# Kernel tuning notes

Hardware: AMD Instinct MI355X
Metric: run time of the kernel (lower is better)

The kernel has to match this reference:

```python
import jax, jax.numpy as jnp
import numpy as np

TAU = 0.5  # config.tau
EPS = 1e-12  # F.normalize eps


def _pair_idx(n_i, hi):
    # all pairs (i, j) with i in [0, n_i), j in (i, hi)
    ii, jj = [], []
    for i in range(n_i):
        js = np.arange(i + 1, hi)
        ii.append(np.full(js.shape, i))
        jj.append(js)
    return np.concatenate(ii), np.concatenate(jj)


def setup_inputs() -> dict:
    key = jax.random.key(0)
    ks = jax.random.split(key, 7)
    B, D, H = 512, 768, 256
    s = 0.02
    return {
        "emb_in": jax.random.normal(ks[0], (B, D), jnp.float32),
        "W1": jax.random.normal(ks[1], (H, 2 * D), jnp.float32) * s,
        "b1": jax.random.normal(ks[2], (H,), jnp.float32) * s,
        "W2": jax.random.normal(ks[3], (H, H), jnp.float32) * s,
        "b2": jax.random.normal(ks[4], (H,), jnp.float32) * s,
        "W3": jax.random.normal(ks[5], (1, H), jnp.float32) * s,
        "b3": jax.random.normal(ks[6], (1,), jnp.float32) * s,
    }


def reference(emb_in, W1, b1, W2, b2, W3, b3):
    B, D = emb_in.shape
    n = B // 4
    m = B // 2

    # L2 normalize rows (torch F.normalize)
    z = emb_in / jnp.maximum(jnp.linalg.norm(emb_in, axis=1, keepdims=True), EPS)
    # cosine similarity matrix [B, B]
    S = z @ z.T

    # ---- ContrastiveLoss (NT-Xent style over first n rows) ----
    logits = S / jnp.asarray(TAU, emb_in.dtype)
    not_diag = 1.0 - jnp.eye(B, dtype=emb_in.dtype)
    denom = jnp.sum(not_diag * jnp.exp(logits), axis=1)  # sum_{k != i} exp(S[i,k]/T)
    log_denom = jnp.log(denom)  # [B]
    ci, cj = _pair_idx(n, n)  # pairs i < j < n
    # loss_ij = -log( exp(S[i,j]/T) / denom_i ) = log_denom[i] - logits[i, j]
    closs_sum = jnp.sum(log_denom[ci] - logits[ci, cj])
    closs = (-2.0 * (n - 1) / n) * closs_sum

    # ---- en_loss: pairwise concat + tiny MLP + BCEWithLogits ----
    ei_np, ej_np = _pair_idx(n, B)  # pairs i in [0,n), j in (i, B)
    ei = jnp.asarray(ei_np)
    ej = jnp.asarray(ej_np)
    labels = (ej_np < m).astype(np.float32)  # first m-(i+1) pairs per i are positives
    labels = jnp.asarray(labels)

    x = jnp.concatenate([z[ei], z[ej]], axis=1)  # [P, 2D]
    h1 = jax.nn.relu(x @ W1.T + b1)              # [P, H]
    h2 = jax.nn.relu(h1 @ W2.T + b2)             # [P, H]
    logit = (h2 @ W3.T + b3)[:, 0]               # [P]

    # BCEWithLogitsLoss (mean), numerically stable form
    bce = jnp.maximum(logit, 0.0) - logit * labels + jnp.log1p(jnp.exp(-jnp.abs(logit)))
    eloss = jnp.mean(bce)

    return closs + eloss
```

## Files before the change

### kernel.cpp

```cpp
#include <hip/hip_runtime.h>
#include <hip/hip_bf16.h>
#include <math.h>

#define B 512
#define D 768
#define H 256
#define NN 128
#define MM 256
#define P_PAIRS 57280
#define NPBLK_P 448

typedef _Float16 f16x8 __attribute__((ext_vector_type(8)));
typedef _Float16 f16x4 __attribute__((ext_vector_type(4)));
typedef float f32x4 __attribute__((ext_vector_type(4)));


__global__ __launch_bounds__(256) void k_prep(const float* __restrict__ emb,
                                              const float* __restrict__ W1,
                                              const float* __restrict__ W2,
                                              _Float16* __restrict__ zH,
                                              _Float16* __restrict__ W1H,
                                              _Float16* __restrict__ W2H) {
    int bx = blockIdx.x;
    int tid = threadIdx.x;
    int w = tid >> 6, lane = tid & 63;

    if (bx < 32) {
        int g = bx;
        __shared__ float invs[16];
        for (int rr = 0; rr < 4; rr++) {
            int row = 16 * g + 4 * w + rr;
            const float* rp = emb + row * D;
            float ss = 0.f;
            #pragma unroll
            for (int it = 0; it < 12; it++) {
                float v = rp[lane + 64 * it];
                ss += v * v;
            }
            #pragma unroll
            for (int m = 1; m <= 32; m <<= 1) ss += __shfl_xor(ss, m);
            if (lane == 0) invs[4 * w + rr] = 1.0f / fmaxf(sqrtf(ss), 1e-12f);
        }
        __syncthreads();
        for (int it = 0; it < 6; it++) {
            int chunk = it * 256 + tid;
            int s = chunk >> 6, lc = chunk & 63;
            int q = lc >> 4, r = lc & 15;
            const float* src = emb + (16 * g + r) * D + 32 * s + 8 * q;
            float inv = invs[r];
            float4 a = *(const float4*)src;
            float4 b = *(const float4*)(src + 4);
            f16x8 o;
            o[0] = (_Float16)(a.x * inv); o[1] = (_Float16)(a.y * inv);
            o[2] = (_Float16)(a.z * inv); o[3] = (_Float16)(a.w * inv);
            o[4] = (_Float16)(b.x * inv); o[5] = (_Float16)(b.y * inv);
            o[6] = (_Float16)(b.z * inv); o[7] = (_Float16)(b.w * inv);
            *(f16x8*)(zH + ((g * 24 + s) * 64 + lc) * 8) = o;
        }
    } else if (bx < 64) {
        int g = bx - 32;
        for (int it = 0; it < 6; it++) {
            int chunk = it * 256 + tid;
            int s = chunk >> 6, lc = chunk & 63;
            int q = lc >> 4, r = lc & 15;
            int n = 16 * g + r;
            const float* src = W1 + (n & 255) * (2 * D) + (n >> 8) * D + 32 * s + 8 * q;
            float4 a = *(const float4*)src;
            float4 b = *(const float4*)(src + 4);
            f16x8 o;
            o[0] = (_Float16)a.x; o[1] = (_Float16)a.y; o[2] = (_Float16)a.z; o[3] = (_Float16)a.w;
            o[4] = (_Float16)b.x; o[5] = (_Float16)b.y; o[6] = (_Float16)b.z; o[7] = (_Float16)b.w;
            *(f16x8*)(W1H + ((g * 24 + s) * 64 + lc) * 8) = o;
        }
    } else {
        int g = bx - 64;
        for (int it = 0; it < 2; it++) {
            int chunk = it * 256 + tid;
            int s = chunk >> 6, lc = chunk & 63;
            int q = lc >> 4, r = lc & 15;
            const float* src = W2 + (16 * g + r) * H + 32 * s + 8 * q;
            float4 a = *(const float4*)src;
            float4 b = *(const float4*)(src + 4);
            f16x8 o;
            o[0] = (_Float16)a.x; o[1] = (_Float16)a.y; o[2] = (_Float16)a.z; o[3] = (_Float16)a.w;
            o[4] = (_Float16)b.x; o[5] = (_Float16)b.y; o[6] = (_Float16)b.z; o[7] = (_Float16)b.w;
            *(f16x8*)(W2H + ((g * 8 + s) * 64 + lc) * 8) = o;
        }
    }
}

__global__ __launch_bounds__(256) void k_uv(const _Float16* __restrict__ zH,
                                            const _Float16* __restrict__ W1H,
                                            const float* __restrict__ b1,
                                            _Float16* __restrict__ Up,
                                            _Float16* __restrict__ Vv) {
    int w = threadIdx.x >> 6;
    int lane = threadIdx.x & 63;
    int r = lane & 15, q = lane >> 4;
    int tile = blockIdx.x * 4 + w;
    int gm = tile >> 4;
    int gnp = tile & 15;

    f32x4 acc[2] = {};
    #pragma unroll 4
    for (int s = 0; s < 24; s++) {
        f16x8 a = *(const f16x8*)(zH + ((gm * 24 + s) * 64 + lane) * 8);
        #pragma unroll
        for (int nt = 0; nt < 2; nt++) {
            f16x8 b = *(const f16x8*)(W1H + (((gnp * 2 + nt) * 24 + s) * 64 + lane) * 8);
            acc[nt] = __builtin_amdgcn_mfma_f32_16x16x32_f16(a, b, acc[nt], 0, 0, 0);
        }
    }
    #pragma unroll
    for (int nt = 0; nt < 2; nt++) {
        int n = (gnp * 2 + nt) * 16 + r;
        float bias = (n < H) ? b1[n] : 0.f;
        #pragma unroll
        for (int rr = 0; rr < 4; rr++) {
            int m = gm * 16 + 4 * q + rr;
            float C = acc[nt][rr] + bias;
            if (n < H) Up[m * H + n] = (_Float16)C;
            else       Vv[m * H + (n - H)] = (_Float16)C;
        }
    }
}

__global__ __launch_bounds__(256, 2) void k_pairs(const _Float16* __restrict__ Up,
                                                  const _Float16* __restrict__ Vv,
                                                  const _Float16* __restrict__ W2H,
                                                  const _Float16* __restrict__ zH,
                                                  const float* __restrict__ b2,
                                                  const float* __restrict__ W3,
                                                  const float* __restrict__ b3,
                                                  float* __restrict__ bcepart,
                                                  float* __restrict__ esp,
                                                  float* __restrict__ slp) {
    int tid = threadIdx.x;
    int w = tid >> 6, lane = tid & 63;
    int r = lane & 15, q = lane >> 4;
    int bx = blockIdx.x;

    if (bx >= NPBLK_P) {
        int t = (bx - NPBLK_P) * 4 + w;
        int gm = t >> 3;
        int slot = t & 7;
        int gn0 = slot * 4;
        f32x4 acc[4] = {};
        #pragma unroll 4
        for (int s = 0; s < 24; s++) {
            f16x8 a = *(const f16x8*)(zH + ((gm * 24 + s) * 64 + lane) * 8);
            #pragma unroll
            for (int nt = 0; nt < 4; nt++) {
                f16x8 b = *(const f16x8*)(zH + (((gn0 + nt) * 24 + s) * 64 + lane) * 8);
                acc[nt] = __builtin_amdgcn_mfma_f32_16x16x32_f16(a, b, acc[nt], 0, 0, 0);
            }
        }
        #pragma unroll
        for (int rr = 0; rr < 4; rr++) {
            int irow = gm * 16 + q * 4 + rr;
            float es = 0.f, sl = 0.f;
            #pragma unroll
            for (int nt = 0; nt < 4; nt++) {
                int kcol = (gn0 + nt) * 16 + r;
                float C = acc[nt][rr];
                if (kcol != irow) es += expf(2.f * C);
                if (kcol > irow && kcol < NN) sl += 2.f * C;
            }
            #pragma unroll
            for (int m = 1; m <= 8; m <<= 1) {
                es += __shfl_xor(es, m);
                sl += __shfl_xor(sl, m);
            }
            if (r == 0) {
                esp[slot * NN + irow] = es;
                slp[slot * NN + irow] = sl;
            }
        }
        return;
    }

    __shared__ _Float16 h1[128][264];
    __shared__ int jj_s[128];
    __shared__ float redbuf[4][128];
    __shared__ float red2[2];

    int p0 = bx * 128;
    if (tid < 128) {
        int p = p0 + tid;
        if (p >= P_PAIRS) p = P_PAIRS - 1;
        float disc = 1046529.f - 8.f * (float)p;
        int i = (int)((1023.f - sqrtf(disc)) * 0.5f);
        if (i < 0) i = 0;
        if (i > NN - 1) i = NN - 1;
        while (i > 0 && i * (1023 - i) / 2 > p) i--;
        while ((i + 1) * (1022 - i) / 2 <= p) i++;
        int j = i + 1 + (p - i * (1023 - i) / 2);
        jj_s[tid] = (i << 16) | j;
    }
    __syncthreads();

    {
        #pragma unroll
        for (int uu = 0; uu < 2; uu++) {
            int u = uu * 256 + tid;
            int row = u >> 2, cq = u & 3;
            int ij = jj_s[row];
            int i = ij >> 16, j = ij & 0xffff;
            const _Float16* up = Up + i * H + 64 * cq;
            const _Float16* vp = Vv + j * H + 64 * cq;
            #pragma unroll
            for (int c8 = 0; c8 < 8; c8++) {
                f16x8 u8 = *(const f16x8*)(up + 8 * c8);
                f16x8 v8 = *(const f16x8*)(vp + 8 * c8);
                f16x8 zero = {};
                f16x8 hv = __builtin_elementwise_max(u8 + v8, zero);
                *(f16x8*)&h1[row][64 * cq + 8 * c8] = hv;
            }
        }
    }
    __syncthreads();

    f32x4 acc[8][4] = {};
    #pragma unroll
    for (int s = 0; s < 8; s++) {
        f16x8 b[4];
        #pragma unroll
        for (int nt = 0; nt < 4; nt++)
            b[nt] = *(const f16x8*)(W2H + (((4 * w + nt) * 8 + s) * 64 + lane) * 8);
        #pragma unroll
        for (int mt = 0; mt < 8; mt++) {
            f16x8 a = *(const f16x8*)&h1[16 * mt + r][32 * s + 8 * q];
            #pragma unroll
            for (int nt = 0; nt < 4; nt++)
                acc[mt][nt] = __builtin_amdgcn_mfma_f32_16x16x32_f16(a, b[nt], acc[mt][nt], 0, 0, 0);
        }
    }

    float b2v[4], w3v[4];
    #pragma unroll
    for (int nt = 0; nt < 4; nt++) {
        int n = 64 * w + 16 * nt + r;
        b2v[nt] = b2[n];
        w3v[nt] = W3[n];
    }
    #pragma unroll
    for (int mt = 0; mt < 8; mt++) {
        float part[4] = {0.f, 0.f, 0.f, 0.f};
        #pragma unroll
        for (int nt = 0; nt < 4; nt++)
            #pragma unroll
            for (int rr = 0; rr < 4; rr++) {
                float h2 = fmaxf(acc[mt][nt][rr] + b2v[nt], 0.f);
                part[rr] += h2 * w3v[nt];
            }
        #pragma unroll
        for (int rr = 0; rr < 4; rr++) {
            float v = part[rr];
            #pragma unroll
            for (int m = 1; m <= 8; m <<= 1) v += __shfl_xor(v, m);
            if (r == 0) redbuf[w][16 * mt + 4 * q + rr] = v;
        }
    }
    __syncthreads();

    if (tid < 128) {
        int p = p0 + tid;
        int j = jj_s[tid] & 0xffff;
        float lsum = 0.f;
        if (p < P_PAIRS) {
            float logit = redbuf[0][tid] + redbuf[1][tid] +
                          redbuf[2][tid] + redbuf[3][tid] + b3[0];
            float label = (j < MM) ? 1.f : 0.f;
            lsum = fmaxf(logit, 0.f) - logit * label + log1pf(expf(-fabsf(logit)));
        }
        #pragma unroll
        for (int off = 32; off > 0; off >>= 1) lsum += __shfl_down(lsum, off);
        if ((tid & 63) == 0) red2[tid >> 6] = lsum;
    }
    __syncthreads();
    if (tid == 0) bcepart[bx] = red2[0] + red2[1];
}

__global__ __launch_bounds__(256) void k_final(const float* __restrict__ esp,
                                               const float* __restrict__ slp,
                                               const float* __restrict__ bcepart,
                                               float* __restrict__ out) {
    __shared__ float red[256];
    int t = threadIdx.x;

    float s = 0.f;
    for (int p = t; p < NPBLK_P; p += 256) s += bcepart[p];
    red[t] = s;
    __syncthreads();
    for (int st = 128; st > 0; st >>= 1) {
        if (t < st) red[t] += red[t + st];
        __syncthreads();
    }
    float bce_total = red[0];
    __syncthreads();

    float v = 0.f;
    if (t < NN) {
        float es = 0.f, sl = 0.f;
        #pragma unroll
        for (int s8 = 0; s8 < 8; s8++) {
            es += esp[s8 * NN + t];
            sl += slp[s8 * NN + t];
        }
        v = (float)(NN - 1 - t) * logf(es) - sl;
    }
    red[t] = v;
    __syncthreads();
    for (int st = 128; st > 0; st >>= 1) {
        if (t < st) red[t] += red[t + st];
        __syncthreads();
    }
    if (t == 0) {
        float closs = (-2.0f * (float)(NN - 1) / (float)NN) * red[0];
        out[0] = closs + bce_total / (float)P_PAIRS;
    }
}

extern "C" void kernel_launch(void* const* d_in, const int* in_sizes, int n_in,
                              void* d_out, int out_size, void* d_ws, size_t ws_size,
                              hipStream_t stream) {
    const float* emb = (const float*)d_in[0];
    const float* W1  = (const float*)d_in[1];
    const float* b1  = (const float*)d_in[2];
    const float* W2  = (const float*)d_in[3];
    const float* b2  = (const float*)d_in[4];
    const float* W3  = (const float*)d_in[5];
    const float* b3  = (const float*)d_in[6];
    float* out = (float*)d_out;

    float* ws = (float*)d_ws;
    float* esp     = ws;
    float* slp     = ws + 1024;
    float* bcepart = ws + 2048;
    _Float16* zH  = (_Float16*)(ws + 2560);
    _Float16* W1H = zH + B * D;
    _Float16* W2H = W1H + 2 * H * D;
    _Float16* Up  = W2H + H * H;
    _Float16* Vv  = Up + B * H;

    k_prep<<<80, 256, 0, stream>>>(emb, W1, W2, zH, W1H, W2H);
    k_uv<<<128, 256, 0, stream>>>(zH, W1H, b1, Up, Vv);
    k_pairs<<<NPBLK_P + 16, 256, 0, stream>>>(Up, Vv, W2H, zH, b2, W3, b3,
                                              bcepart, esp, slp);
    k_final<<<1, 256, 0, stream>>>(esp, slp, bcepart, out);
}
```

Baseline: 101.3 us.

## Fuse fp16 conversion into GEMM loads, move similarity GEMM earlier, fold final reduction

```diff
diff --git a/kernel.cpp b/kernel.cpp
--- a/kernel.cpp
+++ b/kernel.cpp
@@ -11,74 +11,43 @@
 #define NPBLK_P 448
 
 typedef _Float16 f16x8 __attribute__((ext_vector_type(8)));
-typedef _Float16 f16x4 __attribute__((ext_vector_type(4)));
 typedef float f32x4 __attribute__((ext_vector_type(4)));
 
 
-__global__ __launch_bounds__(256) void k_prep(const float* __restrict__ emb,
-                                              const float* __restrict__ W1,
+__global__ __launch_bounds__(256) void k_norm(const float* __restrict__ emb,
                                               const float* __restrict__ W2,
-                                              _Float16* __restrict__ zH,
-                                              _Float16* __restrict__ W1H,
-                                              _Float16* __restrict__ W2H) {
+                                              float* __restrict__ inv,
+                                              _Float16* __restrict__ W2H,
+                                              int* __restrict__ counter) {
     int bx = blockIdx.x;
-    int tid = threadIdx.x;
-    int w = tid >> 6, lane = tid & 63;
-
+    int t = threadIdx.x;
     if (bx < 32) {
-        int g = bx;
-        __shared__ float invs[16];
-        for (int rr = 0; rr < 4; rr++) {
-            int row = 16 * g + 4 * w + rr;
-            const float* rp = emb + row * D;
-            float ss = 0.f;
-            #pragma unroll
-            for (int it = 0; it < 12; it++) {
-                float v = rp[lane + 64 * it];
-                ss += v * v;
-            }
-            #pragma unroll
-            for (int m = 1; m <= 32; m <<= 1) ss += __shfl_xor(ss, m);
-            if (lane == 0) invs[4 * w + rr] = 1.0f / fmaxf(sqrtf(ss), 1e-12f);
-        }
+        __shared__ float ssq[16][17];
+        int row16 = t >> 4, seg = t & 15;
+        const float4* rp = (const float4*)(emb + (16 * bx + row16) * D + seg * 48);
+        float ss = 0.f;
+        #pragma unroll
+        for (int it = 0; it < 12; it++) {
+            float4 v = rp[it];
+            ss += v.x * v.x + v.y * v.y + v.z * v.z + v.w * v.w;
+        }
+        ssq[row16][seg] = ss;
         __syncthreads();
-        for (int it = 0; it < 6; it++) {
-            int chunk = it * 256 + tid;
+        if (t < 16) {
+            float s = 0.f;
+            #pragma unroll
+            for (int k = 0; k < 16; k++) s += ssq[t][k];
+            inv[16 * bx + t] = 1.0f / fmaxf(sqrtf(s), 1e-12f);
+        }
+    } else {
+        int g = bx - 32;
+        if (g == 0 && t == 0) *counter = 0;
+        #pragma unroll
+        for (int it = 0; it < 2; it++) {
+            int chunk = it * 256 + t;
             int s = chunk >> 6, lc = chunk & 63;
-            int q = lc >> 4, r = lc & 15;
-            const float* src = emb + (16 * g + r) * D + 32 * s + 8 * q;
-            float inv = invs[r];
-            float4 a = *(const float4*)src;
-            float4 b = *(const float4*)(src + 4);
-            f16x8 o;
-            o[0] = (_Float16)(a.x * inv); o[1] = (_Float16)(a.y * inv);
-            o[2] = (_Float16)(a.z * inv); o[3] = (_Float16)(a.w * inv);
-            o[4] = (_Float16)(b.x * inv); o[5] = (_Float16)(b.y * inv);
-            o[6] = (_Float16)(b.z * inv); o[7] = (_Float16)(b.w * inv);
-            *(f16x8*)(zH + ((g * 24 + s) * 64 + lc) * 8) = o;
-        }
-    } else if (bx < 64) {
-        int g = bx - 32;
-        for (int it = 0; it < 6; it++) {
-            int chunk = it * 256 + tid;
-            int s = chunk >> 6, lc = chunk & 63;
-            int q = lc >> 4, r = lc & 15;
-            int n = 16 * g + r;
-            const float* src = W1 + (n & 255) * (2 * D) + (n >> 8) * D + 32 * s + 8 * q;
-            float4 a = *(const float4*)src;
-            float4 b = *(const float4*)(src + 4);
-            f16x8 o;
-            o[0] = (_Float16)a.x; o[1] = (_Float16)a.y; o[2] = (_Float16)a.z; o[3] = (_Float16)a.w;
-            o[4] = (_Float16)b.x; o[5] = (_Float16)b.y; o[6] = (_Float16)b.z; o[7] = (_Float16)b.w;
-            *(f16x8*)(W1H + ((g * 24 + s) * 64 + lc) * 8) = o;
-        }
-    } else {
-        int g = bx - 64;
-        for (int it = 0; it < 2; it++) {
-            int chunk = it * 256 + tid;
-            int s = chunk >> 6, lc = chunk & 63;
-            int q = lc >> 4, r = lc & 15;
-            const float* src = W2 + (16 * g + r) * H + 32 * s + 8 * q;
+            int qq = lc >> 4, rr = lc & 15;
+            const float* src = W2 + (16 * g + rr) * H + 32 * s + 8 * qq;
             float4 a = *(const float4*)src;
             float4 b = *(const float4*)(src + 4);
             f16x8 o;
@@ -89,70 +58,100 @@
     }
 }
 
-__global__ __launch_bounds__(256) void k_uv(const _Float16* __restrict__ zH,
-                                            const _Float16* __restrict__ W1H,
-                                            const float* __restrict__ b1,
-                                            _Float16* __restrict__ Up,
-                                            _Float16* __restrict__ Vv) {
+__global__ __launch_bounds__(256) void k_uvsim(const float* __restrict__ emb,
+                                               const float* __restrict__ W1,
+                                               const float* __restrict__ b1,
+                                               const float* __restrict__ inv,
+                                               _Float16* __restrict__ Up,
+                                               _Float16* __restrict__ Vv,
+                                               float* __restrict__ esp,
+                                               float* __restrict__ slp) {
+    int bx = blockIdx.x;
     int w = threadIdx.x >> 6;
     int lane = threadIdx.x & 63;
     int r = lane & 15, q = lane >> 4;
-    int tile = blockIdx.x * 4 + w;
-    int gm = tile >> 4;
-    int gnp = tile & 15;
-
-    f32x4 acc[2] = {};
-    #pragma unroll 4
-    for (int s = 0; s < 24; s++) {
-        f16x8 a = *(const f16x8*)(zH + ((gm * 24 + s) * 64 + lane) * 8);
+
+    if (bx < 128) {
+        int gm = bx >> 2;
+        int gnp = (bx & 3) * 4 + w;
+        float invA = inv[16 * gm + r];
+        const float* ap = emb + (16 * gm + r) * D + 8 * q;
+        const float* wp[2];
         #pragma unroll
         for (int nt = 0; nt < 2; nt++) {
-            f16x8 b = *(const f16x8*)(W1H + (((gnp * 2 + nt) * 24 + s) * 64 + lane) * 8);
-            acc[nt] = __builtin_amdgcn_mfma_f32_16x16x32_f16(a, b, acc[nt], 0, 0, 0);
-        }
-    }
-    #pragma unroll
-    for (int nt = 0; nt < 2; nt++) {
-        int n = (gnp * 2 + nt) * 16 + r;
-        float bias = (n < H) ? b1[n] : 0.f;
-        #pragma unroll
-        for (int rr = 0; rr < 4; rr++) {
-            int m = gm * 16 + 4 * q + rr;
-            float C = acc[nt][rr] + bias;
-            if (n < H) Up[m * H + n] = (_Float16)C;
-            else       Vv[m * H + (n - H)] = (_Float16)C;
-        }
-    }
-}
-
-__global__ __launch_bounds__(256, 2) void k_pairs(const _Float16* __restrict__ Up,
-                                                  const _Float16* __restrict__ Vv,
-                                                  const _Float16* __restrict__ W2H,
-                                                  const _Float16* __restrict__ zH,
-                                                  const float* __restrict__ b2,
-                                                  const float* __restrict__ W3,
-                                                  const float* __restrict__ b3,
-                                                  float* __restrict__ bcepart,
-                                                  float* __restrict__ esp,
-                                                  float* __restrict__ slp) {
-    int tid = threadIdx.x;
-    int w = tid >> 6, lane = tid & 63;
-    int r = lane & 15, q = lane >> 4;
-    int bx = blockIdx.x;
-
-    if (bx >= NPBLK_P) {
-        int t = (bx - NPBLK_P) * 4 + w;
-        int gm = t >> 3;
-        int slot = t & 7;
+            int n = gnp * 32 + nt * 16 + r;
+            wp[nt] = W1 + (n & 255) * (2 * D) + (n >> 8) * D + 8 * q;
+        }
+        f32x4 acc[2] = {};
+        #pragma unroll 2
+        for (int s = 0; s < 24; s++) {
+            float4 a0 = *(const float4*)(ap + 32 * s);
+            float4 a1 = *(const float4*)(ap + 32 * s + 4);
+            f16x8 af;
+            af[0] = (_Float16)(a0.x * invA); af[1] = (_Float16)(a0.y * invA);
+            af[2] = (_Float16)(a0.z * invA); af[3] = (_Float16)(a0.w * invA);
+            af[4] = (_Float16)(a1.x * invA); af[5] = (_Float16)(a1.y * invA);
+            af[6] = (_Float16)(a1.z * invA); af[7] = (_Float16)(a1.w * invA);
+            #pragma unroll
+            for (int nt = 0; nt < 2; nt++) {
+                float4 b0 = *(const float4*)(wp[nt] + 32 * s);
+                float4 b1v = *(const float4*)(wp[nt] + 32 * s + 4);
+                f16x8 bf;
+                bf[0] = (_Float16)b0.x; bf[1] = (_Float16)b0.y;
+                bf[2] = (_Float16)b0.z; bf[3] = (_Float16)b0.w;
+                bf[4] = (_Float16)b1v.x; bf[5] = (_Float16)b1v.y;
+                bf[6] = (_Float16)b1v.z; bf[7] = (_Float16)b1v.w;
+                acc[nt] = __builtin_amdgcn_mfma_f32_16x16x32_f16(af, bf, acc[nt], 0, 0, 0);
+            }
+        }
+        #pragma unroll
+        for (int nt = 0; nt < 2; nt++) {
+            int n = (gnp * 2 + nt) * 16 + r;
+            float bias = (n < H) ? b1[n] : 0.f;
+            #pragma unroll
+            for (int rr = 0; rr < 4; rr++) {
+                int m = gm * 16 + 4 * q + rr;
+                float C = acc[nt][rr] + bias;
+                if (n < H) Up[m * H + n] = (_Float16)C;
+                else       Vv[m * H + (n - H)] = (_Float16)C;
+            }
+        }
+    } else {
+        int sb = bx - 128;
+        int gm = sb >> 1;
+        int slot = (sb & 1) * 4 + w;
         int gn0 = slot * 4;
+        float invA = inv[16 * gm + r];
+        float invB[4];
+        const float* bp[4];
+        #pragma unroll
+        for (int nt = 0; nt < 4; nt++) {
+            int n = (gn0 + nt) * 16 + r;
+            invB[nt] = inv[n];
+            bp[nt] = emb + n * D + 8 * q;
+        }
+        const float* ap = emb + (16 * gm + r) * D + 8 * q;
         f32x4 acc[4] = {};
-        #pragma unroll 4
+        #pragma unroll 2
         for (int s = 0; s < 24; s++) {
-            f16x8 a = *(const f16x8*)(zH + ((gm * 24 + s) * 64 + lane) * 8);
+            float4 a0 = *(const float4*)(ap + 32 * s);
+            float4 a1 = *(const float4*)(ap + 32 * s + 4);
+            f16x8 af;
+            af[0] = (_Float16)(a0.x * invA); af[1] = (_Float16)(a0.y * invA);
+            af[2] = (_Float16)(a0.z * invA); af[3] = (_Float16)(a0.w * invA);
+            af[4] = (_Float16)(a1.x * invA); af[5] = (_Float16)(a1.y * invA);
+            af[6] = (_Float16)(a1.z * invA); af[7] = (_Float16)(a1.w * invA);
             #pragma unroll
             for (int nt = 0; nt < 4; nt++) {
-                f16x8 b = *(const f16x8*)(zH + (((gn0 + nt) * 24 + s) * 64 + lane) * 8);
-                acc[nt] = __builtin_amdgcn_mfma_f32_16x16x32_f16(a, b, acc[nt], 0, 0, 0);
+                float4 b0 = *(const float4*)(bp[nt] + 32 * s);
+                float4 b1v = *(const float4*)(bp[nt] + 32 * s + 4);
+                float ib = invB[nt];
+                f16x8 bf;
+                bf[0] = (_Float16)(b0.x * ib); bf[1] = (_Float16)(b0.y * ib);
+                bf[2] = (_Float16)(b0.z * ib); bf[3] = (_Float16)(b0.w * ib);
+                bf[4] = (_Float16)(b1v.x * ib); bf[5] = (_Float16)(b1v.y * ib);
+                bf[6] = (_Float16)(b1v.z * ib); bf[7] = (_Float16)(b1v.w * ib);
+                acc[nt] = __builtin_amdgcn_mfma_f32_16x16x32_f16(af, bf, acc[nt], 0, 0, 0);
             }
         }
         #pragma unroll
@@ -176,13 +175,30 @@
                 slp[slot * NN + irow] = sl;
             }
         }
-        return;
-    }
-
+    }
+}
+
+__global__ __launch_bounds__(256, 2) void k_pairs(const _Float16* __restrict__ Up,
+                                                  const _Float16* __restrict__ Vv,
+                                                  const _Float16* __restrict__ W2H,
+                                                  const float* __restrict__ b2,
+                                                  const float* __restrict__ W3,
+                                                  const float* __restrict__ b3,
+                                                  const float* __restrict__ esp,
+                                                  const float* __restrict__ slp,
+                                                  float* __restrict__ bcepart,
+                                                  int* __restrict__ counter,
+                                                  float* __restrict__ out) {
     __shared__ _Float16 h1[128][264];
     __shared__ int jj_s[128];
     __shared__ float redbuf[4][128];
     __shared__ float red2[2];
+    __shared__ int islast_s;
+
+    int tid = threadIdx.x;
+    int w = tid >> 6, lane = tid & 63;
+    int r = lane & 15, q = lane >> 4;
+    int bx = blockIdx.x;
 
     int p0 = bx * 128;
     if (tid < 128) {
@@ -199,23 +215,21 @@
     }
     __syncthreads();
 
-    {
-        #pragma unroll
-        for (int uu = 0; uu < 2; uu++) {
-            int u = uu * 256 + tid;
-            int row = u >> 2, cq = u & 3;
-            int ij = jj_s[row];
-            int i = ij >> 16, j = ij & 0xffff;
-            const _Float16* up = Up + i * H + 64 * cq;
-            const _Float16* vp = Vv + j * H + 64 * cq;
-            #pragma unroll
-            for (int c8 = 0; c8 < 8; c8++) {
-                f16x8 u8 = *(const f16x8*)(up + 8 * c8);
-                f16x8 v8 = *(const f16x8*)(vp + 8 * c8);
-                f16x8 zero = {};
-                f16x8 hv = __builtin_elementwise_max(u8 + v8, zero);
-                *(f16x8*)&h1[row][64 * cq + 8 * c8] = hv;
-            }
+    #pragma unroll
+    for (int uu = 0; uu < 2; uu++) {
+        int u = uu * 256 + tid;
+        int row = u >> 2, cq = u & 3;
+        int ij = jj_s[row];
+        int i = ij >> 16, j = ij & 0xffff;
+        const _Float16* up = Up + i * H + 64 * cq;
+        const _Float16* vp = Vv + j * H + 64 * cq;
+        #pragma unroll
+        for (int c8 = 0; c8 < 8; c8++) {
+            f16x8 u8 = *(const f16x8*)(up + 8 * c8);
+            f16x8 v8 = *(const f16x8*)(vp + 8 * c8);
+            f16x8 zero = {};
+            f16x8 hv = __builtin_elementwise_max(u8 + v8, zero);
+            *(f16x8*)&h1[row][64 * cq + 8 * c8] = hv;
         }
     }
     __syncthreads();
@@ -223,16 +237,16 @@
     f32x4 acc[8][4] = {};
     #pragma unroll
     for (int s = 0; s < 8; s++) {
-        f16x8 b[4];
+        f16x8 bb[4];
         #pragma unroll
         for (int nt = 0; nt < 4; nt++)
-            b[nt] = *(const f16x8*)(W2H + (((4 * w + nt) * 8 + s) * 64 + lane) * 8);
+            bb[nt] = *(const f16x8*)(W2H + (((4 * w + nt) * 8 + s) * 64 + lane) * 8);
         #pragma unroll
         for (int mt = 0; mt < 8; mt++) {
             f16x8 a = *(const f16x8*)&h1[16 * mt + r][32 * s + 8 * q];
             #pragma unroll
             for (int nt = 0; nt < 4; nt++)
-                acc[mt][nt] = __builtin_amdgcn_mfma_f32_16x16x32_f16(a, b[nt], acc[mt][nt], 0, 0, 0);
+                acc[mt][nt] = __builtin_amdgcn_mfma_f32_16x16x32_f16(a, bb[nt], acc[mt][nt], 0, 0, 0);
         }
     }
 
@@ -278,46 +292,48 @@
         if ((tid & 63) == 0) red2[tid >> 6] = lsum;
     }
     __syncthreads();
-    if (tid == 0) bcepart[bx] = red2[0] + red2[1];
-}
-
-__global__ __launch_bounds__(256) void k_final(const float* __restrict__ esp,
-                                               const float* __restrict__ slp,
-                                               const float* __restrict__ bcepart,
-                                               float* __restrict__ out) {
-    __shared__ float red[256];
-    int t = threadIdx.x;
-
-    float s = 0.f;
-    for (int p = t; p < NPBLK_P; p += 256) s += bcepart[p];
-    red[t] = s;
-    __syncthreads();
-    for (int st = 128; st > 0; st >>= 1) {
-        if (t < st) red[t] += red[t + st];
+
+    if (tid == 0) {
+        bcepart[bx] = red2[0] + red2[1];
+        __threadfence();
+        int old = atomicAdd(counter, 1);
+        islast_s = (old == NPBLK_P - 1);
+    }
+    __syncthreads();
+    if (islast_s) {
+        __threadfence();
+        float* fred = &redbuf[0][0];
+        float s = 0.f;
+        for (int p = tid; p < NPBLK_P; p += 256) s += bcepart[p];
+        fred[tid] = s;
         __syncthreads();
-    }
-    float bce_total = red[0];
-    __syncthreads();
-
-    float v = 0.f;
-    if (t < NN) {
-        float es = 0.f, sl = 0.f;
-        #pragma unroll
-        for (int s8 = 0; s8 < 8; s8++) {
-            es += esp[s8 * NN + t];
-            sl += slp[s8 * NN + t];
-        }
-        v = (float)(NN - 1 - t) * logf(es) - sl;
-    }
-    red[t] = v;
-    __syncthreads();
-    for (int st = 128; st > 0; st >>= 1) {
-        if (t < st) red[t] += red[t + st];
+        for (int st = 128; st > 0; st >>= 1) {
+            if (tid < st) fred[tid] += fred[tid + st];
+            __syncthreads();
+        }
+        float bce_total = fred[0];
         __syncthreads();
-    }
-    if (t == 0) {
-        float closs = (-2.0f * (float)(NN - 1) / (float)NN) * red[0];
-        out[0] = closs + bce_total / (float)P_PAIRS;
+
+        float v = 0.f;
+        if (tid < NN) {
+            float es = 0.f, sl = 0.f;
+            #pragma unroll
+            for (int s8 = 0; s8 < 8; s8++) {
+                es += esp[s8 * NN + tid];
+                sl += slp[s8 * NN + tid];
+            }
+            v = (float)(NN - 1 - tid) * logf(es) - sl;
+        }
+        fred[tid] = v;
+        __syncthreads();
+        for (int st = 128; st > 0; st >>= 1) {
+            if (tid < st) fred[tid] += fred[tid + st];
+            __syncthreads();
+        }
+        if (tid == 0) {
+            float closs = (-2.0f * (float)(NN - 1) / (float)NN) * fred[0];
+            out[0] = closs + bce_total / (float)P_PAIRS;
+        }
     }
 }
 
@@ -337,15 +353,14 @@
     float* esp     = ws;
     float* slp     = ws + 1024;
     float* bcepart = ws + 2048;
-    _Float16* zH  = (_Float16*)(ws + 2560);
-    _Float16* W1H = zH + B * D;
-    _Float16* W2H = W1H + 2 * H * D;
+    float* inv     = ws + 2560;
+    int*   counter = (int*)(ws + 3072);
+    _Float16* W2H = (_Float16*)(ws + 3136);
     _Float16* Up  = W2H + H * H;
     _Float16* Vv  = Up + B * H;
 
-    k_prep<<<80, 256, 0, stream>>>(emb, W1, W2, zH, W1H, W2H);
-    k_uv<<<128, 256, 0, stream>>>(zH, W1H, b1, Up, Vv);
-    k_pairs<<<NPBLK_P + 16, 256, 0, stream>>>(Up, Vv, W2H, zH, b2, W3, b3,
-                                              bcepart, esp, slp);
-    k_final<<<1, 256, 0, stream>>>(esp, slp, bcepart, out);
+    k_norm<<<48, 256, 0, stream>>>(emb, W2, inv, W2H, counter);
+    k_uvsim<<<144, 256, 0, stream>>>(emb, W1, b1, inv, Up, Vv, esp, slp);
+    k_pairs<<<NPBLK_P, 256, 0, stream>>>(Up, Vv, W2H, b2, W3, b3,
+                                         esp, slp, bcepart, counter, out);
 }
```

New measurement: 133.4 us. +31.7%, slower.

## Fuse final reduction into pairs kernel and rebalance stages across kernels

Applied to the files above, without the earlier changes.

```diff
diff --git a/kernel.cpp b/kernel.cpp
--- a/kernel.cpp
+++ b/kernel.cpp
@@ -11,23 +11,21 @@
 #define NPBLK_P 448
 
 typedef _Float16 f16x8 __attribute__((ext_vector_type(8)));
-typedef _Float16 f16x4 __attribute__((ext_vector_type(4)));
 typedef float f32x4 __attribute__((ext_vector_type(4)));
 
 
 __global__ __launch_bounds__(256) void k_prep(const float* __restrict__ emb,
                                               const float* __restrict__ W1,
-                                              const float* __restrict__ W2,
                                               _Float16* __restrict__ zH,
                                               _Float16* __restrict__ W1H,
-                                              _Float16* __restrict__ W2H) {
+                                              int* __restrict__ counter) {
+    __shared__ float invs[16];
     int bx = blockIdx.x;
     int tid = threadIdx.x;
     int w = tid >> 6, lane = tid & 63;
 
     if (bx < 32) {
         int g = bx;
-        __shared__ float invs[16];
         for (int rr = 0; rr < 4; rr++) {
             int row = 16 * g + 4 * w + rr;
             const float* rp = emb + row * D;
@@ -45,103 +43,82 @@
         for (int it = 0; it < 6; it++) {
             int chunk = it * 256 + tid;
             int s = chunk >> 6, lc = chunk & 63;
-            int q = lc >> 4, r = lc & 15;
-            const float* src = emb + (16 * g + r) * D + 32 * s + 8 * q;
-            float inv = invs[r];
+            int qq = lc >> 4, rr = lc & 15;
+            const float* src = emb + (16 * g + rr) * D + 32 * s + 8 * qq;
+            float inv = invs[rr];
             float4 a = *(const float4*)src;
-            float4 b = *(const float4*)(src + 4);
+            float4 bb = *(const float4*)(src + 4);
             f16x8 o;
             o[0] = (_Float16)(a.x * inv); o[1] = (_Float16)(a.y * inv);
             o[2] = (_Float16)(a.z * inv); o[3] = (_Float16)(a.w * inv);
-            o[4] = (_Float16)(b.x * inv); o[5] = (_Float16)(b.y * inv);
-            o[6] = (_Float16)(b.z * inv); o[7] = (_Float16)(b.w * inv);
+            o[4] = (_Float16)(bb.x * inv); o[5] = (_Float16)(bb.y * inv);
+            o[6] = (_Float16)(bb.z * inv); o[7] = (_Float16)(bb.w * inv);
             *(f16x8*)(zH + ((g * 24 + s) * 64 + lc) * 8) = o;
         }
-    } else if (bx < 64) {
-        int g = bx - 32;
-        for (int it = 0; it < 6; it++) {
+    } else {
+        int g = (bx - 32) >> 1;
+        int h = (bx - 32) & 1;
+        if (bx == 32 && tid == 0) *counter = 0;
+        for (int it = 0; it < 3; it++) {
             int chunk = it * 256 + tid;
-            int s = chunk >> 6, lc = chunk & 63;
-            int q = lc >> 4, r = lc & 15;
-            int n = 16 * g + r;
-            const float* src = W1 + (n & 255) * (2 * D) + (n >> 8) * D + 32 * s + 8 * q;
+            int s = h * 12 + (chunk >> 6);
+            int lc = chunk & 63;
+            int qq = lc >> 4, rr = lc & 15;
+            int n = 16 * g + rr;
+            const float* src = W1 + (n & 255) * (2 * D) + (n >> 8) * D + 32 * s + 8 * qq;
             float4 a = *(const float4*)src;
-            float4 b = *(const float4*)(src + 4);
+            float4 bb = *(const float4*)(src + 4);
             f16x8 o;
             o[0] = (_Float16)a.x; o[1] = (_Float16)a.y; o[2] = (_Float16)a.z; o[3] = (_Float16)a.w;
-            o[4] = (_Float16)b.x; o[5] = (_Float16)b.y; o[6] = (_Float16)b.z; o[7] = (_Float16)b.w;
+            o[4] = (_Float16)bb.x; o[5] = (_Float16)bb.y; o[6] = (_Float16)bb.z; o[7] = (_Float16)bb.w;
             *(f16x8*)(W1H + ((g * 24 + s) * 64 + lc) * 8) = o;
         }
-    } else {
-        int g = bx - 64;
-        for (int it = 0; it < 2; it++) {
-            int chunk = it * 256 + tid;
-            int s = chunk >> 6, lc = chunk & 63;
-            int q = lc >> 4, r = lc & 15;
-            const float* src = W2 + (16 * g + r) * H + 32 * s + 8 * q;
-            float4 a = *(const float4*)src;
-            float4 b = *(const float4*)(src + 4);
-            f16x8 o;
-            o[0] = (_Float16)a.x; o[1] = (_Float16)a.y; o[2] = (_Float16)a.z; o[3] = (_Float16)a.w;
-            o[4] = (_Float16)b.x; o[5] = (_Float16)b.y; o[6] = (_Float16)b.z; o[7] = (_Float16)b.w;
-            *(f16x8*)(W2H + ((g * 8 + s) * 64 + lc) * 8) = o;
-        }
     }
 }
 
-__global__ __launch_bounds__(256) void k_uv(const _Float16* __restrict__ zH,
-                                            const _Float16* __restrict__ W1H,
-                                            const float* __restrict__ b1,
-                                            _Float16* __restrict__ Up,
-                                            _Float16* __restrict__ Vv) {
-    int w = threadIdx.x >> 6;
-    int lane = threadIdx.x & 63;
+__global__ __launch_bounds__(256) void k_uvsim(const _Float16* __restrict__ zH,
+                                               const _Float16* __restrict__ W1H,
+                                               const float* __restrict__ W2,
+                                               const float* __restrict__ b1,
+                                               _Float16* __restrict__ Up,
+                                               _Float16* __restrict__ Vv,
+                                               _Float16* __restrict__ W2H,
+                                               float* __restrict__ esp,
+                                               float* __restrict__ slp) {
+    int bx = blockIdx.x;
+    int tid = threadIdx.x;
+    int w = tid >> 6;
+    int lane = tid & 63;
     int r = lane & 15, q = lane >> 4;
-    int tile = blockIdx.x * 4 + w;
-    int gm = tile >> 4;
-    int gnp = tile & 15;
-
-    f32x4 acc[2] = {};
-    #pragma unroll 4
-    for (int s = 0; s < 24; s++) {
-        f16x8 a = *(const f16x8*)(zH + ((gm * 24 + s) * 64 + lane) * 8);
+
+    if (bx < 128) {
+        int gid = bx * 4 + w;
+        int gm = gid >> 4;
+        int gnp = gid & 15;
+        f32x4 acc[2] = {};
+        #pragma unroll 4
+        for (int s = 0; s < 24; s++) {
+            f16x8 a = *(const f16x8*)(zH + ((gm * 24 + s) * 64 + lane) * 8);
+            #pragma unroll
+            for (int nt = 0; nt < 2; nt++) {
+                f16x8 bb = *(const f16x8*)(W1H + (((gnp * 2 + nt) * 24 + s) * 64 + lane) * 8);
+                acc[nt] = __builtin_amdgcn_mfma_f32_16x16x32_f16(a, bb, acc[nt], 0, 0, 0);
+            }
+        }
         #pragma unroll
         for (int nt = 0; nt < 2; nt++) {
-            f16x8 b = *(const f16x8*)(W1H + (((gnp * 2 + nt) * 24 + s) * 64 + lane) * 8);
-            acc[nt] = __builtin_amdgcn_mfma_f32_16x16x32_f16(a, b, acc[nt], 0, 0, 0);
-        }
-    }
-    #pragma unroll
-    for (int nt = 0; nt < 2; nt++) {
-        int n = (gnp * 2 + nt) * 16 + r;
-        float bias = (n < H) ? b1[n] : 0.f;
-        #pragma unroll
-        for (int rr = 0; rr < 4; rr++) {
-            int m = gm * 16 + 4 * q + rr;
-            float C = acc[nt][rr] + bias;
-            if (n < H) Up[m * H + n] = (_Float16)C;
-            else       Vv[m * H + (n - H)] = (_Float16)C;
-        }
-    }
-}
-
-__global__ __launch_bounds__(256, 2) void k_pairs(const _Float16* __restrict__ Up,
-                                                  const _Float16* __restrict__ Vv,
-                                                  const _Float16* __restrict__ W2H,
-                                                  const _Float16* __restrict__ zH,
-                                                  const float* __restrict__ b2,
-                                                  const float* __restrict__ W3,
-                                                  const float* __restrict__ b3,
-                                                  float* __restrict__ bcepart,
-                                                  float* __restrict__ esp,
-                                                  float* __restrict__ slp) {
-    int tid = threadIdx.x;
-    int w = tid >> 6, lane = tid & 63;
-    int r = lane & 15, q = lane >> 4;
-    int bx = blockIdx.x;
-
-    if (bx >= NPBLK_P) {
-        int t = (bx - NPBLK_P) * 4 + w;
+            int n = (gnp * 2 + nt) * 16 + r;
+            float bias = (n < H) ? b1[n] : 0.f;
+            #pragma unroll
+            for (int rr = 0; rr < 4; rr++) {
+                int m = gm * 16 + 4 * q + rr;
+                float C = acc[nt][rr] + bias;
+                if (n < H) Up[m * H + n] = (_Float16)C;
+                else       Vv[m * H + (n - H)] = (_Float16)C;
+            }
+        }
+    } else if (bx < 144) {
+        int t = (bx - 128) * 4 + w;
         int gm = t >> 3;
         int slot = t & 7;
         int gn0 = slot * 4;
@@ -151,8 +128,8 @@
             f16x8 a = *(const f16x8*)(zH + ((gm * 24 + s) * 64 + lane) * 8);
             #pragma unroll
             for (int nt = 0; nt < 4; nt++) {
-                f16x8 b = *(const f16x8*)(zH + (((gn0 + nt) * 24 + s) * 64 + lane) * 8);
-                acc[nt] = __builtin_amdgcn_mfma_f32_16x16x32_f16(a, b, acc[nt], 0, 0, 0);
+                f16x8 bb = *(const f16x8*)(zH + (((gn0 + nt) * 24 + s) * 64 + lane) * 8);
+                acc[nt] = __builtin_amdgcn_mfma_f32_16x16x32_f16(a, bb, acc[nt], 0, 0, 0);
             }
         }
         #pragma unroll
@@ -176,13 +153,45 @@
                 slp[slot * NN + irow] = sl;
             }
         }
-        return;
-    }
-
+    } else {
+        int g = bx - 144;
+        #pragma unroll
+        for (int it = 0; it < 2; it++) {
+            int chunk = it * 256 + tid;
+            int s = chunk >> 6, lc = chunk & 63;
+            int qq = lc >> 4, rr = lc & 15;
+            const float* src = W2 + (16 * g + rr) * H + 32 * s + 8 * qq;
+            float4 a = *(const float4*)src;
+            float4 bb = *(const float4*)(src + 4);
+            f16x8 o;
+            o[0] = (_Float16)a.x; o[1] = (_Float16)a.y; o[2] = (_Float16)a.z; o[3] = (_Float16)a.w;
+            o[4] = (_Float16)bb.x; o[5] = (_Float16)bb.y; o[6] = (_Float16)bb.z; o[7] = (_Float16)bb.w;
+            *(f16x8*)(W2H + ((g * 8 + s) * 64 + lc) * 8) = o;
+        }
+    }
+}
+
+__global__ __launch_bounds__(256, 2) void k_pairs(const _Float16* __restrict__ Up,
+                                                  const _Float16* __restrict__ Vv,
+                                                  const _Float16* __restrict__ W2H,
+                                                  const float* __restrict__ b2,
+                                                  const float* __restrict__ W3,
+                                                  const float* __restrict__ b3,
+                                                  const float* __restrict__ esp,
+                                                  const float* __restrict__ slp,
+                                                  float* __restrict__ bcepart,
+                                                  int* __restrict__ counter,
+                                                  float* __restrict__ out) {
     __shared__ _Float16 h1[128][264];
     __shared__ int jj_s[128];
     __shared__ float redbuf[4][128];
     __shared__ float red2[2];
+    __shared__ int islast_s;
+
+    int tid = threadIdx.x;
+    int w = tid >> 6, lane = tid & 63;
+    int r = lane & 15, q = lane >> 4;
+    int bx = blockIdx.x;
 
     int p0 = bx * 128;
     if (tid < 128) {
@@ -199,23 +208,21 @@
     }
     __syncthreads();
 
-    {
-        #pragma unroll
-        for (int uu = 0; uu < 2; uu++) {
-            int u = uu * 256 + tid;
-            int row = u >> 2, cq = u & 3;
-            int ij = jj_s[row];
-            int i = ij >> 16, j = ij & 0xffff;
-            const _Float16* up = Up + i * H + 64 * cq;
-            const _Float16* vp = Vv + j * H + 64 * cq;
-            #pragma unroll
-            for (int c8 = 0; c8 < 8; c8++) {
-                f16x8 u8 = *(const f16x8*)(up + 8 * c8);
-                f16x8 v8 = *(const f16x8*)(vp + 8 * c8);
-                f16x8 zero = {};
-                f16x8 hv = __builtin_elementwise_max(u8 + v8, zero);
-                *(f16x8*)&h1[row][64 * cq + 8 * c8] = hv;
-            }
+    #pragma unroll
+    for (int uu = 0; uu < 2; uu++) {
+        int u = uu * 256 + tid;
+        int row = u >> 2, cq = u & 3;
+        int ij = jj_s[row];
+        int i = ij >> 16, j = ij & 0xffff;
+        const _Float16* up = Up + i * H + 64 * cq;
+        const _Float16* vp = Vv + j * H + 64 * cq;
+        #pragma unroll
+        for (int c8 = 0; c8 < 8; c8++) {
+            f16x8 u8 = *(const f16x8*)(up + 8 * c8);
+            f16x8 v8 = *(const f16x8*)(vp + 8 * c8);
+            f16x8 zero = {};
+            f16x8 hv = __builtin_elementwise_max(u8 + v8, zero);
+            *(f16x8*)&h1[row][64 * cq + 8 * c8] = hv;
         }
     }
     __syncthreads();
@@ -223,16 +230,16 @@
     f32x4 acc[8][4] = {};
     #pragma unroll
     for (int s = 0; s < 8; s++) {
-        f16x8 b[4];
+        f16x8 bb[4];
         #pragma unroll
         for (int nt = 0; nt < 4; nt++)
-            b[nt] = *(const f16x8*)(W2H + (((4 * w + nt) * 8 + s) * 64 + lane) * 8);
+            bb[nt] = *(const f16x8*)(W2H + (((4 * w + nt) * 8 + s) * 64 + lane) * 8);
         #pragma unroll
         for (int mt = 0; mt < 8; mt++) {
             f16x8 a = *(const f16x8*)&h1[16 * mt + r][32 * s + 8 * q];
             #pragma unroll
             for (int nt = 0; nt < 4; nt++)
-                acc[mt][nt] = __builtin_amdgcn_mfma_f32_16x16x32_f16(a, b[nt], acc[mt][nt], 0, 0, 0);
+                acc[mt][nt] = __builtin_amdgcn_mfma_f32_16x16x32_f16(a, bb[nt], acc[mt][nt], 0, 0, 0);
         }
     }
 
@@ -278,46 +285,48 @@
         if ((tid & 63) == 0) red2[tid >> 6] = lsum;
     }
     __syncthreads();
-    if (tid == 0) bcepart[bx] = red2[0] + red2[1];
-}
-
-__global__ __launch_bounds__(256) void k_final(const float* __restrict__ esp,
-                                               const float* __restrict__ slp,
-                                               const float* __restrict__ bcepart,
-                                               float* __restrict__ out) {
-    __shared__ float red[256];
-    int t = threadIdx.x;
-
-    float s = 0.f;
-    for (int p = t; p < NPBLK_P; p += 256) s += bcepart[p];
-    red[t] = s;
-    __syncthreads();
-    for (int st = 128; st > 0; st >>= 1) {
-        if (t < st) red[t] += red[t + st];
+
+    if (tid == 0) {
+        bcepart[bx] = red2[0] + red2[1];
+        __threadfence();
+        int old = atomicAdd(counter, 1);
+        islast_s = (old == NPBLK_P - 1);
+    }
+    __syncthreads();
+    if (islast_s) {
+        __threadfence();
+        float* fred = &redbuf[0][0];
+        float s = 0.f;
+        for (int p = tid; p < NPBLK_P; p += 256) s += bcepart[p];
+        fred[tid] = s;
         __syncthreads();
-    }
-    float bce_total = red[0];
-    __syncthreads();
-
-    float v = 0.f;
-    if (t < NN) {
-        float es = 0.f, sl = 0.f;
-        #pragma unroll
-        for (int s8 = 0; s8 < 8; s8++) {
-            es += esp[s8 * NN + t];
-            sl += slp[s8 * NN + t];
-        }
-        v = (float)(NN - 1 - t) * logf(es) - sl;
-    }
-    red[t] = v;
-    __syncthreads();
-    for (int st = 128; st > 0; st >>= 1) {
-        if (t < st) red[t] += red[t + st];
+        for (int st = 128; st > 0; st >>= 1) {
+            if (tid < st) fred[tid] += fred[tid + st];
+            __syncthreads();
+        }
+        float bce_total = fred[0];
         __syncthreads();
-    }
-    if (t == 0) {
-        float closs = (-2.0f * (float)(NN - 1) / (float)NN) * red[0];
-        out[0] = closs + bce_total / (float)P_PAIRS;
+
+        float v = 0.f;
+        if (tid < NN) {
+            float es = 0.f, sl = 0.f;
+            #pragma unroll
+            for (int s8 = 0; s8 < 8; s8++) {
+                es += esp[s8 * NN + tid];
+                sl += slp[s8 * NN + tid];
+            }
+            v = (float)(NN - 1 - tid) * logf(es) - sl;
+        }
+        fred[tid] = v;
+        __syncthreads();
+        for (int st = 128; st > 0; st >>= 1) {
+            if (tid < st) fred[tid] += fred[tid + st];
+            __syncthreads();
+        }
+        if (tid == 0) {
+            float closs = (-2.0f * (float)(NN - 1) / (float)NN) * fred[0];
+            out[0] = closs + bce_total / (float)P_PAIRS;
+        }
     }
 }
 
@@ -337,15 +346,15 @@
     float* esp     = ws;
     float* slp     = ws + 1024;
     float* bcepart = ws + 2048;
-    _Float16* zH  = (_Float16*)(ws + 2560);
+    int*   counter = (int*)(ws + 2560);
+    _Float16* zH  = (_Float16*)(ws + 3072);
     _Float16* W1H = zH + B * D;
     _Float16* W2H = W1H + 2 * H * D;
     _Float16* Up  = W2H + H * H;
     _Float16* Vv  = Up + B * H;
 
-    k_prep<<<80, 256, 0, stream>>>(emb, W1, W2, zH, W1H, W2H);
-    k_uv<<<128, 256, 0, stream>>>(zH, W1H, b1, Up, Vv);
-    k_pairs<<<NPBLK_P + 16, 256, 0, stream>>>(Up, Vv, W2H, zH, b2, W3, b3,
-                                              bcepart, esp, slp);
-    k_final<<<1, 256, 0, stream>>>(esp, slp, bcepart, out);
+    k_prep<<<96, 256, 0, stream>>>(emb, W1, zH, W1H, counter);
+    k_uvsim<<<160, 256, 0, stream>>>(zH, W1H, W2, b1, Up, Vv, W2H, esp, slp);
+    k_pairs<<<NPBLK_P, 256, 0, stream>>>(Up, Vv, W2H, b2, W3, b3,
+                                         esp, slp, bcepart, counter, out);
 }
```

After: 111.1 us. 1.1x slower.
